# Performance work log

Measured on AMD Instinct MI355X. Metric: run time of the kernel, lower is better.

## Reference

```python
import jax, jax.numpy as jnp
from jax import lax
import numpy as np
import math

T, B, F = 512, 256, 256  # num_steps, batch, input_size == hidden_size
H = F


def setup_inputs() -> dict:
    key = jax.random.key(0)
    ks = jax.random.split(key, 20)
    stdv = 1.0 / math.sqrt(H)

    def u(k, n):
        return jax.random.uniform(k, (n,), jnp.float32, -stdv, stdv)

    X = jax.random.normal(ks[0], (T, B, F), jnp.float32)
    Mask = (jax.random.uniform(ks[1], (T, B, F)) < 0.7).astype(jnp.float32)
    Delta = jax.random.uniform(ks[2], (T, B, F), jnp.float32)

    return {
        "X": X, "Mask": Mask, "Delta": Delta,
        "x_mean": u(ks[3], F),
        "w_dg_x": u(ks[4], F), "b_dg_x": u(ks[5], F),
        "w_dg_h": u(ks[6], H), "b_dg_h": u(ks[7], H),
        "w_xz": u(ks[8], F), "u_hz": u(ks[9], H), "b_z": u(ks[10], H),
        "w_xr": u(ks[11], F), "u_hr": u(ks[12], H), "b_r": u(ks[13], H),
        "w_xh": u(ks[14], F), "u_hh": u(ks[15], H), "v_mh": u(ks[16], F),
        "b_h": u(ks[17], H),
    }


def reference(X, Mask, Delta, x_mean, w_dg_x, b_dg_x, w_dg_h, b_dg_h,
              w_xz, u_hz, b_z, w_xr, u_hr, b_r, w_xh, u_hh, v_mh, b_h):
    batch = X.shape[1]

    def step(h, inp):
        x, m, d = inp  # each [B, F]
        gamma_x = jnp.exp(-jnp.maximum(0.0, w_dg_x * d + b_dg_x))
        gamma_h = jnp.exp(-jnp.maximum(0.0, w_dg_h * d + b_dg_h))
        x = m * x + (1.0 - m) * (gamma_x * x + (1.0 - gamma_x) * x_mean)
        h = gamma_h * h
        z = jax.nn.sigmoid(w_xz * x + u_hz * h + b_z)
        r = jax.nn.sigmoid(w_xr * x + u_hr * h + b_r)
        h_tilde = jnp.tanh(w_xh * x + u_hh * (r * h) + v_mh * m + b_h)
        h = (1.0 - z) * h + z * h_tilde
        return h, h

    h0 = jnp.zeros((batch, H), X.dtype)
    _, hs = lax.scan(step, h0, (X, Mask, Delta))  # hs: [T, B, H]
    hidden_states = jnp.transpose(hs, (1, 0, 2))  # [B, T, H]
    return hidden_states, hidden_states[:, -1, :]
```

## Files before the change

kernel.cpp:

```cpp
#include <hip/hip_runtime.h>
#include <math.h>


#define TT 512
#define BB 256
#define FF 256
#define BF (BB * FF)
#define CH 8
#define NCH (TT / CH)

__device__ __forceinline__ float fast_sigmoid(float x) {
    return __builtin_amdgcn_rcpf(1.0f + __expf(-x));
}
__device__ __forceinline__ float fast_tanh(float x) {
    return fmaf(-2.0f, __builtin_amdgcn_rcpf(1.0f + __expf(2.0f * x)), 1.0f);
}

typedef __attribute__((address_space(1))) const void gconst_void;
typedef __attribute__((address_space(3))) void lds_void;

__device__ __forceinline__ void gload_lds4(const float* g, float* l) {
    __builtin_amdgcn_global_load_lds((gconst_void*)g, (lds_void*)l, 4, 0, 0);
}

#define VMWAIT(N)                                                   \
    do {                                                            \
        asm volatile("s_waitcnt vmcnt(" #N ")" ::: "memory");       \
        __builtin_amdgcn_sched_barrier(0);                          \
    } while (0)

__global__ __launch_bounds__(256, 1) void grud_kernel(
    const float* __restrict__ X, const float* __restrict__ Mask,
    const float* __restrict__ Delta,
    const float* __restrict__ x_mean,
    const float* __restrict__ w_dg_x, const float* __restrict__ b_dg_x,
    const float* __restrict__ w_dg_h, const float* __restrict__ b_dg_h,
    const float* __restrict__ w_xz, const float* __restrict__ u_hz,
    const float* __restrict__ b_z,
    const float* __restrict__ w_xr, const float* __restrict__ u_hr,
    const float* __restrict__ b_r,
    const float* __restrict__ w_xh, const float* __restrict__ u_hh,
    const float* __restrict__ v_mh, const float* __restrict__ b_h,
    float* __restrict__ out)
{
    __shared__ float lds[4][2][3][CH][64];

    const int tid = threadIdx.x;
    const int w   = tid >> 6;
    const int ln  = tid & 63;
    const int b   = blockIdx.x;

    const size_t base = (size_t)b * FF + tid;
    const float* __restrict__ px = X     + base;
    const float* __restrict__ pm = Mask  + base;
    const float* __restrict__ pd = Delta + base;
    float* __restrict__ ob = out + (size_t)b * TT * FF + tid;

    const float xm  = x_mean[tid];
    const float wdx = w_dg_x[tid], bdx = b_dg_x[tid];
    const float wdh = w_dg_h[tid], bdh = b_dg_h[tid];
    const float wxz = w_xz[tid],   uhz = u_hz[tid], bz = b_z[tid];
    const float wxr = w_xr[tid],   uhr = u_hr[tid], br = b_r[tid];
    const float wxh = w_xh[tid],   uhh = u_hh[tid];
    const float vmh = v_mh[tid],   bh  = b_h[tid];

    asm volatile("" :: "v"(xm), "v"(wdx), "v"(bdx), "v"(wdh), "v"(bdh),
                       "v"(wxz), "v"(uhz), "v"(bz), "v"(wxr), "v"(uhr),
                       "v"(br), "v"(wxh), "v"(uhh), "v"(vmh), "v"(bh));
    float h = 0.0f;

    auto issuec = [&](int buf, int c) {
        const size_t o = (size_t)c * CH * BF;
        #pragma unroll
        for (int s = 0; s < CH; ++s)
            gload_lds4(px + o + (size_t)s * BF, &lds[w][buf][0][s][0]);
        #pragma unroll
        for (int s = 0; s < CH; ++s)
            gload_lds4(pm + o + (size_t)s * BF, &lds[w][buf][1][s][0]);
        #pragma unroll
        for (int s = 0; s < CH; ++s)
            gload_lds4(pd + o + (size_t)s * BF, &lds[w][buf][2][s][0]);
        __builtin_amdgcn_sched_barrier(0);
    };

    auto computec = [&](int buf, int c) {
        float* op = ob + (size_t)c * CH * FF;
        #pragma unroll
        for (int s = 0; s < CH; ++s) {
            float x = lds[w][buf][0][s][ln];
            float m = lds[w][buf][1][s][ln];
            float d = lds[w][buf][2][s][ln];
            float gx = __expf(-fmaxf(0.0f, fmaf(wdx, d, bdx)));
            float gh = __expf(-fmaxf(0.0f, fmaf(wdh, d, bdh)));
            float xhat = fmaf(gx, x, (1.0f - gx) * xm);
            x = fmaf(m, x, (1.0f - m) * xhat);
            h = gh * h;
            float z  = fast_sigmoid(fmaf(wxz, x, fmaf(uhz, h, bz)));
            float r  = fast_sigmoid(fmaf(wxr, x, fmaf(uhr, h, br)));
            float ht = fast_tanh(fmaf(wxh, x, fmaf(uhh, r * h, fmaf(vmh, m, bh))));
            h = fmaf(z, ht - h, h);
            __builtin_nontemporal_store(h, op + (size_t)s * FF);
        }
    };

    issuec(0, 0);
    issuec(1, 1);
    VMWAIT(24);
    computec(0, 0);
    issuec(0, 2);

    for (int c = 1; c <= NCH - 3; ++c) {
        VMWAIT(32);
        computec(c & 1, c);
        issuec(c & 1, c + 2);
    }

    VMWAIT(32);
    computec(0, NCH - 2);
    VMWAIT(8);
    computec(1, NCH - 1);

    out[(size_t)BB * TT * FF + (size_t)b * FF + tid] = h;
}

extern "C" void kernel_launch(void* const* d_in, const int* in_sizes, int n_in,
                              void* d_out, int out_size, void* d_ws, size_t ws_size,
                              hipStream_t stream) {
    const float* X      = (const float*)d_in[0];
    const float* Mask   = (const float*)d_in[1];
    const float* Delta  = (const float*)d_in[2];
    const float* x_mean = (const float*)d_in[3];
    const float* w_dg_x = (const float*)d_in[4];
    const float* b_dg_x = (const float*)d_in[5];
    const float* w_dg_h = (const float*)d_in[6];
    const float* b_dg_h = (const float*)d_in[7];
    const float* w_xz   = (const float*)d_in[8];
    const float* u_hz   = (const float*)d_in[9];
    const float* b_z    = (const float*)d_in[10];
    const float* w_xr   = (const float*)d_in[11];
    const float* u_hr   = (const float*)d_in[12];
    const float* b_r    = (const float*)d_in[13];
    const float* w_xh   = (const float*)d_in[14];
    const float* u_hh   = (const float*)d_in[15];
    const float* v_mh   = (const float*)d_in[16];
    const float* b_h    = (const float*)d_in[17];
    float* out = (float*)d_out;

    grud_kernel<<<BB, 256, 0, stream>>>(
        X, Mask, Delta, x_mean, w_dg_x, b_dg_x, w_dg_h, b_dg_h,
        w_xz, u_hz, b_z, w_xr, u_hr, b_r, w_xh, u_hh, v_mh, b_h, out);
}
```

Measured before the change: 426.7 us.

## Use 16-byte global-to-LDS loads with a shared five-slot prefetch ring

```diff
diff --git a/kernel.cpp b/kernel.cpp
--- a/kernel.cpp
+++ b/kernel.cpp
@@ -8,6 +8,7 @@
 #define BF (BB * FF)
 #define CH 8
 #define NCH (TT / CH)
+#define NB 5
 
 __device__ __forceinline__ float fast_sigmoid(float x) {
     return __builtin_amdgcn_rcpf(1.0f + __expf(-x));
@@ -19,13 +20,19 @@
 typedef __attribute__((address_space(1))) const void gconst_void;
 typedef __attribute__((address_space(3))) void lds_void;
 
-__device__ __forceinline__ void gload_lds4(const float* g, float* l) {
-    __builtin_amdgcn_global_load_lds((gconst_void*)g, (lds_void*)l, 4, 0, 0);
+__device__ __forceinline__ void gload_lds16(const float* g, float* l) {
+    __builtin_amdgcn_global_load_lds((gconst_void*)g, (lds_void*)l, 16, 0, 0);
 }
 
 #define VMWAIT(N)                                                   \
     do {                                                            \
         asm volatile("s_waitcnt vmcnt(" #N ")" ::: "memory");       \
+        __builtin_amdgcn_sched_barrier(0);                          \
+    } while (0)
+
+#define SBAR()                                                      \
+    do {                                                            \
+        __builtin_amdgcn_s_barrier();                               \
         __builtin_amdgcn_sched_barrier(0);                          \
     } while (0)
 
@@ -43,17 +50,18 @@
     const float* __restrict__ v_mh, const float* __restrict__ b_h,
     float* __restrict__ out)
 {
-    __shared__ float lds[4][2][3][CH][64];
+    __shared__ float lds[NB][3][CH][FF];
 
     const int tid = threadIdx.x;
     const int w   = tid >> 6;
     const int ln  = tid & 63;
     const int b   = blockIdx.x;
 
-    const size_t base = (size_t)b * FF + tid;
-    const float* __restrict__ px = X     + base;
-    const float* __restrict__ pm = Mask  + base;
-    const float* __restrict__ pd = Delta + base;
+    const size_t rb = (size_t)b * FF + 4 * (size_t)ln;
+    const float* __restrict__ gx = X     + rb;
+    const float* __restrict__ gm = Mask  + rb;
+    const float* __restrict__ gd = Delta + rb;
+
     float* __restrict__ ob = out + (size_t)b * TT * FF + tid;
 
     const float xm  = x_mean[tid];
@@ -69,56 +77,59 @@
                        "v"(br), "v"(wxh), "v"(uhh), "v"(vmh), "v"(bh));
     float h = 0.0f;
 
-    auto issuec = [&](int buf, int c) {
-        const size_t o = (size_t)c * CH * BF;
+    auto issuec = [&](int c, int slot) {
+        const size_t t0 = (size_t)c * CH;
         #pragma unroll
-        for (int s = 0; s < CH; ++s)
-            gload_lds4(px + o + (size_t)s * BF, &lds[w][buf][0][s][0]);
-        #pragma unroll
-        for (int s = 0; s < CH; ++s)
-            gload_lds4(pm + o + (size_t)s * BF, &lds[w][buf][1][s][0]);
-        #pragma unroll
-        for (int s = 0; s < CH; ++s)
-            gload_lds4(pd + o + (size_t)s * BF, &lds[w][buf][2][s][0]);
+        for (int j = 0; j < 2; ++j) {
+            const int s = 2 * w + j;
+            const size_t off = (t0 + (size_t)s) * BF;
+            gload_lds16(gx + off, &lds[slot][0][s][0]);
+            gload_lds16(gm + off, &lds[slot][1][s][0]);
+            gload_lds16(gd + off, &lds[slot][2][s][0]);
+        }
         __builtin_amdgcn_sched_barrier(0);
     };
 
-    auto computec = [&](int buf, int c) {
+    auto computec = [&](int c, int slot) {
         float* op = ob + (size_t)c * CH * FF;
         #pragma unroll
         for (int s = 0; s < CH; ++s) {
-            float x = lds[w][buf][0][s][ln];
-            float m = lds[w][buf][1][s][ln];
-            float d = lds[w][buf][2][s][ln];
-            float gx = __expf(-fmaxf(0.0f, fmaf(wdx, d, bdx)));
-            float gh = __expf(-fmaxf(0.0f, fmaf(wdh, d, bdh)));
-            float xhat = fmaf(gx, x, (1.0f - gx) * xm);
+            float x = lds[slot][0][s][tid];
+            float m = lds[slot][1][s][tid];
+            float d = lds[slot][2][s][tid];
+            float gxx = __expf(-fmaxf(0.0f, fmaf(wdx, d, bdx)));
+            float ghh = __expf(-fmaxf(0.0f, fmaf(wdh, d, bdh)));
+            float xhat = fmaf(gxx, x, (1.0f - gxx) * xm);
             x = fmaf(m, x, (1.0f - m) * xhat);
-            h = gh * h;
+            h = ghh * h;
             float z  = fast_sigmoid(fmaf(wxz, x, fmaf(uhz, h, bz)));
             float r  = fast_sigmoid(fmaf(wxr, x, fmaf(uhr, h, br)));
             float ht = fast_tanh(fmaf(wxh, x, fmaf(uhh, r * h, fmaf(vmh, m, bh))));
             h = fmaf(z, ht - h, h);
             __builtin_nontemporal_store(h, op + (size_t)s * FF);
         }
+        __builtin_amdgcn_sched_barrier(0);
     };
 
-    issuec(0, 0);
-    issuec(1, 1);
-    VMWAIT(24);
-    computec(0, 0);
-    issuec(0, 2);
+    issuec(0, 0); issuec(1, 1); issuec(2, 2); issuec(3, 3);
 
-    for (int c = 1; c <= NCH - 3; ++c) {
-        VMWAIT(32);
-        computec(c & 1, c);
-        issuec(c & 1, c + 2);
+    VMWAIT(18); SBAR(); computec(0, 0); issuec(4, 4);
+    VMWAIT(26); SBAR(); computec(1, 1); issuec(5, 0);
+    VMWAIT(34); SBAR(); computec(2, 2); issuec(6, 1);
+
+    int cs = 3, is_ = 2;
+    for (int c = 3; c <= NCH - 5; ++c) {
+        VMWAIT(42); SBAR();
+        computec(c, cs);
+        issuec(c + 4, is_);
+        cs  = (cs  + 1 == NB) ? 0 : cs  + 1;
+        is_ = (is_ + 1 == NB) ? 0 : is_ + 1;
     }
 
-    VMWAIT(32);
-    computec(0, NCH - 2);
-    VMWAIT(8);
-    computec(1, NCH - 1);
+    VMWAIT(42); SBAR(); computec(60, 0);
+    VMWAIT(36); SBAR(); computec(61, 1);
+    VMWAIT(30); SBAR(); computec(62, 2);
+    VMWAIT(24); SBAR(); computec(63, 3);
 
     out[(size_t)BB * TT * FF + (size_t)b * FF + tid] = h;
 }
```

Result: no change. 427.9 us (+0.3%).
